# Performance work log

Measured on AMD Instinct MI355X. Metric: run time of the kernel, lower is better.

The kernel has to match this reference:

```python
import jax, jax.numpy as jnp
import numpy as np

NUM_COMPONENTS = 4
HEADS = 16


def setup_inputs() -> dict:
    key = jax.random.key(0)
    ks = jax.random.split(key, 7)
    BC, S, D = 8, 4096, 1024      # batch_times_comp = batch(2) * num_components(4)
    Se, De = 256, 2048            # encoder seq len, encoder hidden dim
    sc = 0.02                     # keep linear outputs in a sane range
    return {
        "hidden_states": jax.random.normal(ks[0], (BC, S, D), jnp.float32),
        "encoder_hidden_states": jax.random.normal(ks[1], (BC, Se, De), jnp.float32),
        "Wq": jax.random.normal(ks[2], (D, D), jnp.float32) * sc,
        "Wk": jax.random.normal(ks[3], (De, D), jnp.float32) * sc,
        "Wv": jax.random.normal(ks[4], (De, D), jnp.float32) * sc,
        "Wo": jax.random.normal(ks[5], (D, D), jnp.float32) * sc,
        "bo": jnp.zeros((D,), jnp.float32),
    }


def reference(hidden_states, encoder_hidden_states, Wq, Wk, Wv, Wo, bo):
    C, H = NUM_COMPONENTS, HEADS
    BC, S, D = hidden_states.shape
    Se = encoder_hidden_states.shape[1]
    B = BC // C
    dh = D // H
    scale = dh ** -0.5  # attn.scale (learn_temperature=False)

    # projections -> [BC, H, S(e), dh]
    q = (hidden_states @ Wq).reshape(BC, S, H, dh).transpose(0, 2, 1, 3)
    k = (encoder_hidden_states @ Wk).reshape(BC, Se, H, dh).transpose(0, 2, 1, 3)
    v = (encoder_hidden_states @ Wv).reshape(BC, Se, H, dh).transpose(0, 2, 1, 3)

    # dense scores [BC, H, S, Se]
    scores = jnp.einsum("bhsd,bhtd->bhst", q, k) * scale
    # softmax over the COMPONENT axis (dim 0 after the 5D view)
    scores5 = scores.reshape(C, B, H, S, Se)
    w = jax.nn.softmax(scores5, axis=0)  # [C, B, H, S, Se]

    # compositional (negative) entropy, summed over components -> [B, H, S, Se]
    compositional_entropy = (w * jnp.log(w)).sum(axis=0)

    # rescale and attend
    w = (w * (C / Se)).reshape(BC, H, S, Se)
    out = jnp.einsum("bhst,bhtd->bhsd", w, v)
    out = out.transpose(0, 2, 1, 3).reshape(BC, S, D)

    # to_out[0] linear (+bias), to_out[1] dropout = identity at eval,
    # residual connection, rescale_output_factor = 1
    out = out @ Wo + bo + hidden_states
    return out, compositional_entropy
```

## Files before the change

### kernel.cpp

```cpp
#include <hip/hip_runtime.h>

typedef unsigned short u16;
typedef __bf16 bf16x4 __attribute__((ext_vector_type(4)));
typedef __bf16 bf16x8 __attribute__((ext_vector_type(8)));
typedef float f32x4 __attribute__((ext_vector_type(4)));
typedef u16 u16x4 __attribute__((ext_vector_type(4)));
typedef u16 u16x8 __attribute__((ext_vector_type(8)));

#define AS1P(p) ((__attribute__((address_space(1))) void*)(unsigned long long)(p))
#define AS3P(p) ((__attribute__((address_space(3))) void*)(unsigned long long)(p))
#define MFMA16(a, b, c) __builtin_amdgcn_mfma_f32_16x16x32_bf16((a), (b), (c), 0, 0, 0)

__device__ __forceinline__ u16 f2b(float x) { return __builtin_bit_cast(u16, (__bf16)x); }
__device__ __forceinline__ float b2f(u16 u) {
  return __builtin_bit_cast(float, (unsigned)u << 16);
}

__global__ __launch_bounds__(256) void cvt_f32_bf16(const float* __restrict__ in,
                                                    u16* __restrict__ out, int n4) {
  int stride = gridDim.x * blockDim.x;
  for (int i = blockIdx.x * blockDim.x + threadIdx.x; i < n4; i += stride) {
    f32x4 v = *(const f32x4*)(in + (long)i * 4);
    u16x4 o;
    o[0] = f2b(v[0]); o[1] = f2b(v[1]); o[2] = f2b(v[2]); o[3] = f2b(v[3]);
    *(u16x4*)(out + (long)i * 4) = o;
  }
}

__global__ __launch_bounds__(256) void wtrans(const float* __restrict__ W,
                                              u16* __restrict__ Wt, int K, int N) {
  __shared__ float tile[32][33];
  int nbk = K >> 5;
  int bk = blockIdx.x % nbk;
  int bn = blockIdx.x / nbk;
  int tx = threadIdx.x & 31, ty = threadIdx.x >> 5;
#pragma unroll
  for (int i = 0; i < 32; i += 8)
    tile[ty + i][tx] = W[(long)(bk * 32 + ty + i) * N + bn * 32 + tx];
  __syncthreads();
#pragma unroll
  for (int i = 0; i < 32; i += 8)
    Wt[(long)(bn * 32 + ty + i) * K + bk * 32 + tx] = f2b(tile[tx][ty + i]);
}

__global__ __launch_bounds__(256) void vtrans(const u16* __restrict__ kvb,
                                              u16* __restrict__ vt) {
  __shared__ u16 tile[32][33];
  int bt = blockIdx.x & 7;
  int bd = (blockIdx.x >> 3) & 31;
  int bc = blockIdx.x >> 8;
  int tx = threadIdx.x & 31, ty = threadIdx.x >> 5;
  const long ob = (long)bc * 1024 * 256;
  const float RS = 1.0f / 64.0f;
#pragma unroll
  for (int i = 0; i < 32; i += 8)
    tile[ty + i][tx] =
        kvb[((long)bc * 256 + bt * 32 + ty + i) * 2048 + 1024 + bd * 32 + tx];
  __syncthreads();
#pragma unroll
  for (int i = 0; i < 32; i += 8)
    vt[ob + (long)(bd * 32 + ty + i) * 256 + bt * 32 + tx] =
        f2b(b2f(tile[tx][ty + i]) * RS);
}

__global__ __launch_bounds__(256) void kfrag_build(const u16* __restrict__ kvb,
                                                   u16* __restrict__ kfrag) {
  int wv = ((int)blockIdx.x << 2) + (threadIdx.x >> 6);
  int lane = threadIdx.x & 63, lr = lane & 15, lg = lane >> 4;
  int ks = wv & 1, tsl = (wv >> 1) & 1, c = (wv >> 2) & 3;
  int ch = (wv >> 4) & 7, h = (wv >> 7) & 15, b = (wv >> 11) & 1;
  const u16* src = kvb + ((long)(c * 2 + b) * 256 + ch * 32 + tsl * 16 + lr) * 2048 +
                   h * 64 + ks * 32 + lg * 8;
  *(bf16x8*)(kfrag + (long)wv * 512 + lane * 8) = *(const bf16x8*)src;
}

__global__ __launch_bounds__(256) void vfrag_build(const u16* __restrict__ vtb,
                                                   u16* __restrict__ vfrag) {
  int wv = ((int)blockIdx.x << 2) + (threadIdx.x >> 6);
  int lane = threadIdx.x & 63, lr = lane & 15, lg = lane >> 4;
  int dsu = wv & 3, c = (wv >> 2) & 3;
  int ch = (wv >> 4) & 7, h = (wv >> 7) & 15, b = (wv >> 11) & 1;
  const u16* src = vtb + ((long)(c * 2 + b) * 1024 + h * 64 + dsu * 16 + lr) * 256 +
                   ch * 32 + lg * 8;
  *(bf16x8*)(vfrag + (long)wv * 512 + lane * 8) = *(const bf16x8*)src;
}

__global__ __launch_bounds__(256) void gemm_bt(
    const u16* __restrict__ A, const u16* __restrict__ Bt,
    u16* __restrict__ outb, int M, int N, int K, float ascale) {
  __shared__ u16 lA[128 * 64];
  __shared__ u16 lB[128 * 64];
  const int tid = threadIdx.x;
  const int lane = tid & 63;
  const int wid = tid >> 6;
  const int wm = wid >> 1, wn = wid & 1;
  const int lr = lane & 15, lg = lane >> 4;

  int bid = (int)blockIdx.x;
  int nwg = (int)gridDim.x;
  if ((nwg & 7) == 0) bid = (bid & 7) * (nwg >> 3) + (bid >> 3);

  const int nbn = N >> 7;
  const int bm = bid / nbn;
  const int bn = bid % nbn;
  const long arow0 = (long)bm * 128;
  const long brow0 = (long)bn * 128;

  f32x4 acc[4][4] = {};

  const int srow = tid >> 3;
  const int scol = tid & 7;

  for (int k0 = 0; k0 < K; k0 += 64) {
#pragma unroll
    for (int i = 0; i < 4; ++i) {
      int row = i * 32 + srow;
      int kc = scol ^ (row & 7);
      __builtin_amdgcn_global_load_lds(AS1P(A + (arow0 + row) * K + k0 + kc * 8),
                                       AS3P(lA + i * 2048 + (tid & ~63) * 8), 16, 0, 0);
    }
#pragma unroll
    for (int i = 0; i < 4; ++i) {
      int row = i * 32 + srow;
      int kc = scol ^ (row & 7);
      __builtin_amdgcn_global_load_lds(AS1P(Bt + (brow0 + row) * K + k0 + kc * 8),
                                       AS3P(lB + i * 2048 + (tid & ~63) * 8), 16, 0, 0);
    }
    asm volatile("s_waitcnt vmcnt(0)" ::: "memory");
    __syncthreads();

#pragma unroll
    for (int ks = 0; ks < 2; ++ks) {
      bf16x8 af[4], bfr[4];
#pragma unroll
      for (int m = 0; m < 4; ++m) {
        int row = wm * 64 + m * 16 + lr;
        int off = row * 128 + ks * 64 + lg * 16;
        off ^= (row & 7) << 4;
        af[m] = *(const bf16x8*)((const char*)lA + off);
      }
#pragma unroll
      for (int n = 0; n < 4; ++n) {
        int row = wn * 64 + n * 16 + lr;
        int off = row * 128 + ks * 64 + lg * 16;
        off ^= (row & 7) << 4;
        bfr[n] = *(const bf16x8*)((const char*)lB + off);
      }
#pragma unroll
      for (int m = 0; m < 4; ++m)
#pragma unroll
        for (int n = 0; n < 4; ++n)
          acc[m][n] = MFMA16(af[m], bfr[n], acc[m][n]);
    }
    __syncthreads();
  }

#pragma unroll
  for (int m = 0; m < 4; ++m)
#pragma unroll
    for (int n = 0; n < 4; ++n) {
      long col = brow0 + wn * 64 + n * 16 + lr;
#pragma unroll
      for (int r = 0; r < 4; ++r) {
        long row = arow0 + wm * 64 + m * 16 + lg * 4 + r;
        outb[row * N + col] = f2b(acc[m][n][r] * ascale);
      }
    }
}

template <int MODE>
__global__ __launch_bounds__(512, 2) void gemm256(
    const u16* __restrict__ A, const u16* __restrict__ Bt,
    u16* __restrict__ outb, float* __restrict__ outf,
    const float* __restrict__ bias, const float* __restrict__ resid,
    int M, int N, int K, float ascale) {
  __shared__ u16 lds[2][2][256 * 64];
  const int tid = threadIdx.x;
  const int lane = tid & 63;
  const int wid = tid >> 6;
  const int wm = wid >> 2;
  const int wn = wid & 3;
  const int lr = lane & 15, lg = lane >> 4;

  int bid = (int)blockIdx.x;
  int nwg = (int)gridDim.x;
  bid = (bid & 7) * (nwg >> 3) + (bid >> 3);

  const int nbn = N >> 8;
  const int bm = bid / nbn;
  const int bn = bid % nbn;
  const long arow0 = (long)bm * 256;
  const long brow0 = (long)bn * 256;

  f32x4 acc[8][4] = {};

  const int srow = tid >> 3;
  const int scol = tid & 7;
  const int nt = K >> 6;

#define STAGE256(bf, t)                                                                \
  do {                                                                                 \
    int k0_ = (t) << 6;                                                                \
    _Pragma("unroll") for (int i = 0; i < 4; ++i) {                                    \
      int row = i * 64 + srow;                                                         \
      int kc = scol ^ (row & 7);                                                       \
      __builtin_amdgcn_global_load_lds(AS1P(A + (arow0 + row) * K + k0_ + kc * 8),     \
                                       AS3P(&lds[bf][0][0] + i * 4096 + (tid & ~63) * 8), \
                                       16, 0, 0);                                      \
    }                                                                                  \
    _Pragma("unroll") for (int i = 0; i < 4; ++i) {                                    \
      int row = i * 64 + srow;                                                         \
      int kc = scol ^ (row & 7);                                                       \
      __builtin_amdgcn_global_load_lds(AS1P(Bt + (brow0 + row) * K + k0_ + kc * 8),    \
                                       AS3P(&lds[bf][1][0] + i * 4096 + (tid & ~63) * 8), \
                                       16, 0, 0);                                      \
    }                                                                                  \
  } while (0)

#define COMPUTE256(bf)                                                                 \
  do {                                                                                 \
    _Pragma("unroll") for (int ks = 0; ks < 2; ++ks) {                                 \
      bf16x8 af[8], bfr[4];                                                            \
      _Pragma("unroll") for (int m = 0; m < 8; ++m) {                                  \
        int row = wm * 128 + m * 16 + lr;                                              \
        int off = row * 128 + ks * 64 + lg * 16;                                       \
        off ^= (row & 7) << 4;                                                         \
        af[m] = *(const bf16x8*)((const char*)&lds[bf][0][0] + off);                   \
      }                                                                                \
      _Pragma("unroll") for (int n = 0; n < 4; ++n) {                                  \
        int row = wn * 64 + n * 16 + lr;                                               \
        int off = row * 128 + ks * 64 + lg * 16;                                       \
        off ^= (row & 7) << 4;                                                         \
        bfr[n] = *(const bf16x8*)((const char*)&lds[bf][1][0] + off);                  \
      }                                                                                \
      _Pragma("unroll") for (int m = 0; m < 8; ++m)                                    \
          _Pragma("unroll") for (int n = 0; n < 4; ++n)                                \
              acc[m][n] = MFMA16(af[m], bfr[n], acc[m][n]);                            \
    }                                                                                  \
  } while (0)

  STAGE256(0, 0);
  asm volatile("s_waitcnt vmcnt(0)" ::: "memory");
  __syncthreads();
  int cur = 0;
  for (int t = 0; t < nt - 1; ++t) {
    STAGE256(cur ^ 1, t + 1);
    COMPUTE256(cur);
    asm volatile("s_waitcnt vmcnt(0)" ::: "memory");
    __syncthreads();
    cur ^= 1;
  }
  COMPUTE256(cur);

#pragma unroll
  for (int m = 0; m < 8; ++m)
#pragma unroll
    for (int n = 0; n < 4; ++n) {
      long col = brow0 + wn * 64 + n * 16 + lr;
#pragma unroll
      for (int r = 0; r < 4; ++r) {
        long row = arow0 + wm * 128 + m * 16 + lg * 4 + r;
        float v = acc[m][n][r];
        if (MODE == 1) {
          long idx = row * N + col;
          outf[idx] = v + bias[col] + resid[idx];
        } else {
          outb[row * N + col] = f2b(v * ascale);
        }
      }
    }
#undef STAGE256
#undef COMPUTE256
}

__global__ __launch_bounds__(256, 1) void attn_fused(
    const u16* __restrict__ q,
    const u16* __restrict__ kfrag,
    const u16* __restrict__ vfrag,
    u16* __restrict__ attn,
    float* __restrict__ ent) {
  const int B = 2, H = 16, S = 4096, Se = 256, D = 1024;
  __shared__ u16 ldsP[4 * 2304];
  const int tid = threadIdx.x;
  const int lane = tid & 63, wid = tid >> 6;
  const int lr = lane & 15, lg = lane >> 4;
  int bid = (int)blockIdx.x;
  bid = (bid & 7) * 256 + (bid >> 3);
  const int sblk = bid & 63;
  const int h = (bid >> 6) & 15;
  const int b = bid >> 10;
  const int s0 = sblk * 64 + wid * 16;

  u16* Pw = ldsP + wid * 2304;

  bf16x8 qf[4][2];
#pragma unroll
  for (int c = 0; c < 4; ++c)
#pragma unroll
    for (int ks = 0; ks < 2; ++ks)
      qf[c][ks] = *(const bf16x8*)(q + ((c * B + b) * (long)S + s0 + lr) * D +
                                   h * 64 + ks * 32 + lg * 8);

  const u16* kbh = kfrag + (long)(b * 16 + h) * 65536 + lane * 8;
  const u16* vbh = vfrag + (long)(b * 16 + h) * 65536 + lane * 8;
  float* entp = ent + ((long)(b * H + h) * S + s0 + lg * 4) * Se + lr;

  const float LN2 = 0.69314718056f;

  f32x4 oacc[4][4] = {};

  bf16x8 kf[16];
#pragma unroll
  for (int i = 0; i < 16; ++i) kf[i] = *(const bf16x8*)(kbh + (i << 9));

#pragma unroll
  for (int ch = 0; ch < 8; ++ch) {
    const u16* vc = vbh + ch * 8192;
    bf16x8 vf[16];
#pragma unroll
    for (int i = 0; i < 16; ++i) vf[i] = *(const bf16x8*)(vc + (i << 9));
    bf16x8 kfn[16];
    if (ch < 7) {
      const u16* kn = kbh + (ch + 1) * 8192;
#pragma unroll
      for (int i = 0; i < 16; ++i) kfn[i] = *(const bf16x8*)(kn + (i << 9));
    }
    __builtin_amdgcn_sched_barrier(0);

    f32x4 sacc[4][2] = {};
#pragma unroll
    for (int c = 0; c < 4; ++c)
#pragma unroll
      for (int tsl = 0; tsl < 2; ++tsl)
#pragma unroll
        for (int ks = 0; ks < 2; ++ks)
          sacc[c][tsl] = MFMA16(qf[c][ks], kf[c * 4 + tsl * 2 + ks], sacc[c][tsl]);

#pragma unroll
    for (int tsl = 0; tsl < 2; ++tsl) {
#pragma unroll
      for (int r = 0; r < 4; ++r) {
        float t0 = sacc[0][tsl][r];
        float t1 = sacc[1][tsl][r];
        float t2 = sacc[2][tsl][r];
        float t3 = sacc[3][tsl][r];
        float e0 = __builtin_amdgcn_exp2f(t0);
        float e1 = __builtin_amdgcn_exp2f(t1);
        float e2 = __builtin_amdgcn_exp2f(t2);
        float e3 = __builtin_amdgcn_exp2f(t3);
        float sum = (e0 + e1) + (e2 + e3);
        float inv = __builtin_amdgcn_rcpf(sum);
        float l2s = __builtin_amdgcn_logf(sum);
        float w0 = e0 * inv, w1 = e1 * inv, w2 = e2 * inv, w3 = e3 * inv;
        float entv = (w0 * t0 + w1 * t1 + w2 * t2 + w3 * t3 - l2s) * LN2;
        __builtin_nontemporal_store(entv, entp + r * Se + ch * 32 + tsl * 16);
        int pof = (lg * 4 + r) * 36 + tsl * 16 + lr;
        Pw[0 * 576 + pof] = f2b(w0);
        Pw[1 * 576 + pof] = f2b(w1);
        Pw[2 * 576 + pof] = f2b(w2);
        Pw[3 * 576 + pof] = f2b(w3);
      }
    }

#pragma unroll
    for (int c = 0; c < 4; ++c) {
      union { bf16x4 hh[2]; bf16x8 v; } pu;
      pu.hh[0] = *(const bf16x4*)(Pw + c * 576 + lr * 36 + lg * 8);
      pu.hh[1] = *(const bf16x4*)(Pw + c * 576 + lr * 36 + lg * 8 + 4);
      bf16x8 pf = pu.v;
#pragma unroll
      for (int dsu = 0; dsu < 4; ++dsu)
        oacc[c][dsu] = MFMA16(pf, vf[c * 4 + dsu], oacc[c][dsu]);
    }

    if (ch < 7) {
#pragma unroll
      for (int i = 0; i < 16; ++i) kf[i] = kfn[i];
    }
  }

#pragma unroll
  for (int c = 0; c < 4; ++c)
#pragma unroll
    for (int dsu = 0; dsu < 4; ++dsu)
#pragma unroll
      for (int r = 0; r < 4; ++r) {
        int s = s0 + lg * 4 + r;
        attn[((c * B + b) * (long)S + s) * D + h * 64 + dsu * 16 + lr] =
            f2b(oacc[c][dsu][r]);
      }
}

extern "C" void kernel_launch(void* const* d_in, const int* in_sizes, int n_in,
                              void* d_out, int out_size, void* d_ws, size_t ws_size,
                              hipStream_t stream) {
  const float* hs  = (const float*)d_in[0];
  const float* ehs = (const float*)d_in[1];
  const float* Wq  = (const float*)d_in[2];
  const float* Wk  = (const float*)d_in[3];
  const float* Wv  = (const float*)d_in[4];
  const float* Wo  = (const float*)d_in[5];
  const float* bo  = (const float*)d_in[6];
  float* out = (float*)d_out;
  float* ent = out + (size_t)8 * 4096 * 1024;

  char* ws = (char*)d_ws;
  u16* hsb   = (u16*)(ws);
  u16* ehsb  = (u16*)(ws + 67108864);
  u16* kfrag = (u16*)(ws + 67108864);
  u16* vfrag = (u16*)(ws + 71303168);
  u16* wqT   = (u16*)(ws + 75497472);
  u16* wkT   = (u16*)(ws + 77594624);
  u16* wvT   = (u16*)(ws + 81788928);
  u16* woT   = (u16*)(ws + 85983232);
  u16* qb    = (u16*)(ws + 88080384);
  u16* kvb   = (u16*)(ws + 155189248);
  u16* vtb   = (u16*)(ws + 163577856);

  const float QSCALE = 0.125f * 1.44269504f;

  cvt_f32_bf16<<<2048, 256, 0, stream>>>(hs, hsb, (8 * 4096 * 1024) / 4);
  cvt_f32_bf16<<<512, 256, 0, stream>>>(ehs, ehsb, (8 * 256 * 2048) / 4);
  wtrans<<<1024, 256, 0, stream>>>(Wq, wqT, 1024, 1024);
  wtrans<<<2048, 256, 0, stream>>>(Wk, wkT, 2048, 1024);
  wtrans<<<2048, 256, 0, stream>>>(Wv, wvT, 2048, 1024);
  wtrans<<<1024, 256, 0, stream>>>(Wo, woT, 1024, 1024);
  gemm256<0><<<(32768 / 256) * (1024 / 256), 512, 0, stream>>>(
      hsb, wqT, qb, nullptr, nullptr, nullptr, 32768, 1024, 1024, QSCALE);
  gemm_bt<<<(2048 / 128) * (2048 / 128), 256, 0, stream>>>(
      ehsb, wkT, kvb, 2048, 2048, 2048, 1.0f);
  vtrans<<<2048, 256, 0, stream>>>(kvb, vtb);
  kfrag_build<<<1024, 256, 0, stream>>>(kvb, kfrag);
  vfrag_build<<<1024, 256, 0, stream>>>(vtb, vfrag);
  attn_fused<<<2048, 256, 0, stream>>>(qb, kfrag, vfrag, hsb, ent);
  gemm256<1><<<(32768 / 256) * (1024 / 256), 512, 0, stream>>>(
      hsb, woT, nullptr, out, bo, hs, 32768, 1024, 1024, 1.0f);
}
```

Baseline: 412.8 us.

## Split gemm256 K-tiles into half-stages with finer-grained LDS pipelining

Restructures the 256x256 GEMM main loop so each 64-wide K tile is staged as two 32-wide halves in separate LDS slots. Fragments for one half are read while the next half is prefetched, and partial vmcnt waits with raw s_barrier replace the full drain and __syncthreads. MFMA bursts are also wrapped in s_setprio to favour matrix issue. The aim is to hide global-to-LDS latency inside the loop, at the cost of more barriers per tile and fragile wait-count accounting.

```diff
diff --git a/kernel.cpp b/kernel.cpp
--- a/kernel.cpp
+++ b/kernel.cpp
@@ -174,7 +174,7 @@
     u16* __restrict__ outb, float* __restrict__ outf,
     const float* __restrict__ bias, const float* __restrict__ resid,
     int M, int N, int K, float ascale) {
-  __shared__ u16 lds[2][2][256 * 64];
+  __shared__ u16 lds[2][2][2][8192];
   const int tid = threadIdx.x;
   const int lane = tid & 63;
   const int wid = tid >> 6;
@@ -193,64 +193,103 @@
   const long brow0 = (long)bn * 256;
 
   f32x4 acc[8][4] = {};
-
-  const int srow = tid >> 3;
-  const int scol = tid & 7;
   const int nt = K >> 6;
 
-#define STAGE256(bf, t)                                                                \
+  const int strow = tid >> 2;
+  const int sslot0 = tid & 3;
+
+#define STAGEH(buf, ks, t)                                                             \
   do {                                                                                 \
-    int k0_ = (t) << 6;                                                                \
-    _Pragma("unroll") for (int i = 0; i < 4; ++i) {                                    \
-      int row = i * 64 + srow;                                                         \
-      int kc = scol ^ (row & 7);                                                       \
-      __builtin_amdgcn_global_load_lds(AS1P(A + (arow0 + row) * K + k0_ + kc * 8),     \
-                                       AS3P(&lds[bf][0][0] + i * 4096 + (tid & ~63) * 8), \
-                                       16, 0, 0);                                      \
-    }                                                                                  \
-    _Pragma("unroll") for (int i = 0; i < 4; ++i) {                                    \
-      int row = i * 64 + srow;                                                         \
-      int kc = scol ^ (row & 7);                                                       \
-      __builtin_amdgcn_global_load_lds(AS1P(Bt + (brow0 + row) * K + k0_ + kc * 8),    \
-                                       AS3P(&lds[bf][1][0] + i * 4096 + (tid & ~63) * 8), \
-                                       16, 0, 0);                                      \
+    const int k0_ = ((t) << 6) + ((ks) << 5);                                          \
+    _Pragma("unroll") for (int i = 0; i < 2; ++i) {                                    \
+      int row = i * 128 + strow;                                                       \
+      int ss = sslot0 ^ (row & 3);                     \
+      __builtin_amdgcn_global_load_lds(                                                \
+          AS1P(A + (arow0 + row) * K + k0_ + ss * 8),                                  \
+          AS3P(&lds[buf][ks][0][0] + i * 4096 + (tid & ~63) * 8), 16, 0, 0);           \
+      __builtin_amdgcn_global_load_lds(                                                \
+          AS1P(Bt + (brow0 + row) * K + k0_ + ss * 8),                                 \
+          AS3P(&lds[buf][ks][1][0] + i * 4096 + (tid & ~63) * 8), 16, 0, 0);           \
     }                                                                                  \
   } while (0)
 
-#define COMPUTE256(bf)                                                                 \
+#define LOADFRAGS(buf, ks)                                                             \
   do {                                                                                 \
-    _Pragma("unroll") for (int ks = 0; ks < 2; ++ks) {                                 \
-      bf16x8 af[8], bfr[4];                                                            \
-      _Pragma("unroll") for (int m = 0; m < 8; ++m) {                                  \
-        int row = wm * 128 + m * 16 + lr;                                              \
-        int off = row * 128 + ks * 64 + lg * 16;                                       \
-        off ^= (row & 7) << 4;                                                         \
-        af[m] = *(const bf16x8*)((const char*)&lds[bf][0][0] + off);                   \
-      }                                                                                \
-      _Pragma("unroll") for (int n = 0; n < 4; ++n) {                                  \
-        int row = wn * 64 + n * 16 + lr;                                               \
-        int off = row * 128 + ks * 64 + lg * 16;                                       \
-        off ^= (row & 7) << 4;                                                         \
-        bfr[n] = *(const bf16x8*)((const char*)&lds[bf][1][0] + off);                  \
-      }                                                                                \
-      _Pragma("unroll") for (int m = 0; m < 8; ++m)                                    \
-          _Pragma("unroll") for (int n = 0; n < 4; ++n)                                \
-              acc[m][n] = MFMA16(af[m], bfr[n], acc[m][n]);                            \
+    const u16* bA = &lds[buf][ks][0][0];                                               \
+    const u16* bB = &lds[buf][ks][1][0];                                               \
+    _Pragma("unroll") for (int m = 0; m < 8; ++m) {                                    \
+      int row = wm * 128 + m * 16 + lr;                                                \
+      af[m] = *(const bf16x8*)(bA + row * 32 + (lg ^ (row & 3)) * 8);                  \
+    }                                                                                  \
+    _Pragma("unroll") for (int n = 0; n < 4; ++n) {                                    \
+      int row = wn * 64 + n * 16 + lr;                                                 \
+      bfr[n] = *(const bf16x8*)(bB + row * 32 + (lg ^ (row & 3)) * 8);                 \
     }                                                                                  \
   } while (0)
 
-  STAGE256(0, 0);
-  asm volatile("s_waitcnt vmcnt(0)" ::: "memory");
-  __syncthreads();
-  int cur = 0;
+#define DOMFMA()                                                                       \
+  do {                                                                                 \
+    __builtin_amdgcn_s_setprio(1);                                                     \
+    _Pragma("unroll") for (int m = 0; m < 8; ++m)                                      \
+        _Pragma("unroll") for (int n = 0; n < 4; ++n)                                  \
+            acc[m][n] = MFMA16(af[m], bfr[n], acc[m][n]);                              \
+    __builtin_amdgcn_s_setprio(0);                                                     \
+  } while (0)
+
+  STAGEH(0, 0, 0);
+  STAGEH(0, 1, 0);
+  STAGEH(1, 0, 1);
+  asm volatile("s_waitcnt vmcnt(8)" ::: "memory");
+  __builtin_amdgcn_s_barrier();
+  __builtin_amdgcn_sched_barrier(0);
+
   for (int t = 0; t < nt - 1; ++t) {
-    STAGE256(cur ^ 1, t + 1);
-    COMPUTE256(cur);
-    asm volatile("s_waitcnt vmcnt(0)" ::: "memory");
-    __syncthreads();
-    cur ^= 1;
+    const int cb = t & 1, nb = cb ^ 1;
+    {
+      bf16x8 af[8], bfr[4];
+      LOADFRAGS(cb, 0);
+      STAGEH(nb, 1, t + 1);
+      asm volatile("s_waitcnt vmcnt(8)" ::: "memory");
+      __builtin_amdgcn_s_barrier();
+      __builtin_amdgcn_sched_barrier(0);
+      DOMFMA();
+      __builtin_amdgcn_s_barrier();
+      __builtin_amdgcn_sched_barrier(0);
+    }
+    {
+      bf16x8 af[8], bfr[4];
+      LOADFRAGS(cb, 1);
+      if (t + 2 < nt) {
+        STAGEH(cb, 0, t + 2);
+        asm volatile("s_waitcnt vmcnt(8)" ::: "memory");
+      } else {
+        asm volatile("s_waitcnt vmcnt(4)" ::: "memory");
+      }
+      __builtin_amdgcn_s_barrier();
+      __builtin_amdgcn_sched_barrier(0);
+      DOMFMA();
+      __builtin_amdgcn_s_barrier();
+      __builtin_amdgcn_sched_barrier(0);
+    }
   }
-  COMPUTE256(cur);
+  {
+    const int cb = (nt - 1) & 1;
+    {
+      bf16x8 af[8], bfr[4];
+      LOADFRAGS(cb, 0);
+      asm volatile("s_waitcnt vmcnt(0)" ::: "memory");
+      __builtin_amdgcn_s_barrier();
+      __builtin_amdgcn_sched_barrier(0);
+      DOMFMA();
+      __builtin_amdgcn_s_barrier();
+      __builtin_amdgcn_sched_barrier(0);
+    }
+    {
+      bf16x8 af[8], bfr[4];
+      LOADFRAGS(cb, 1);
+      DOMFMA();
+    }
+  }
 
 #pragma unroll
   for (int m = 0; m < 8; ++m)
@@ -269,8 +308,9 @@
         }
       }
     }
-#undef STAGE256
-#undef COMPUTE256
+#undef STAGEH
+#undef LOADFRAGS
+#undef DOMFMA
 }
 
 __global__ __launch_bounds__(256, 1) void attn_fused(
```

Measured after the change: 420.1 us. No clear change (+1.8%).

## Double-buffer K/V fragments in attention and read residual from bf16 copy

Applied to the files above, without the earlier changes.

The attention kernel now prefetches both the K and V fragments of the next chunk into ping-pong register buffers, through a fully unrolled macro, instead of loading V for the current chunk just before use. The goal is to hide V load latency behind the score and softmax work. The output projection now reads the residual from the bf16 copy of hidden_states instead of the fp32 input, which halves that read traffic, and it stores the fp32 output with nontemporal stores. Attention output is written in place over the q buffer. The trade-offs are much higher register pressure in the attention kernel and lower precision in the residual add.

```diff
diff --git a/kernel.cpp b/kernel.cpp
--- a/kernel.cpp
+++ b/kernel.cpp
@@ -172,7 +172,7 @@
 __global__ __launch_bounds__(512, 2) void gemm256(
     const u16* __restrict__ A, const u16* __restrict__ Bt,
     u16* __restrict__ outb, float* __restrict__ outf,
-    const float* __restrict__ bias, const float* __restrict__ resid,
+    const float* __restrict__ bias, const u16* __restrict__ residb,
     int M, int N, int K, float ascale) {
   __shared__ u16 lds[2][2][256 * 64];
   const int tid = threadIdx.x;
@@ -263,7 +263,7 @@
         float v = acc[m][n][r];
         if (MODE == 1) {
           long idx = row * N + col;
-          outf[idx] = v + bias[col] + resid[idx];
+          __builtin_nontemporal_store(v + bias[col] + b2f(residb[idx]), outf + idx);
         } else {
           outb[row * N + col] = f2b(v * ascale);
         }
@@ -274,10 +274,10 @@
 }
 
 __global__ __launch_bounds__(256, 1) void attn_fused(
-    const u16* __restrict__ q,
+    const u16* q,
     const u16* __restrict__ kfrag,
     const u16* __restrict__ vfrag,
-    u16* __restrict__ attn,
+    u16* attnout,
     float* __restrict__ ent) {
   const int B = 2, H = 16, S = 4096, Se = 256, D = 1024;
   __shared__ u16 ldsP[4 * 2304];
@@ -309,75 +309,71 @@
 
   f32x4 oacc[4][4] = {};
 
-  bf16x8 kf[16];
-#pragma unroll
-  for (int i = 0; i < 16; ++i) kf[i] = *(const bf16x8*)(kbh + (i << 9));
-
-#pragma unroll
-  for (int ch = 0; ch < 8; ++ch) {
-    const u16* vc = vbh + ch * 8192;
-    bf16x8 vf[16];
-#pragma unroll
-    for (int i = 0; i < 16; ++i) vf[i] = *(const bf16x8*)(vc + (i << 9));
-    bf16x8 kfn[16];
-    if (ch < 7) {
-      const u16* kn = kbh + (ch + 1) * 8192;
-#pragma unroll
-      for (int i = 0; i < 16; ++i) kfn[i] = *(const bf16x8*)(kn + (i << 9));
-    }
-    __builtin_amdgcn_sched_barrier(0);
-
-    f32x4 sacc[4][2] = {};
-#pragma unroll
-    for (int c = 0; c < 4; ++c)
-#pragma unroll
-      for (int tsl = 0; tsl < 2; ++tsl)
-#pragma unroll
-        for (int ks = 0; ks < 2; ++ks)
-          sacc[c][tsl] = MFMA16(qf[c][ks], kf[c * 4 + tsl * 2 + ks], sacc[c][tsl]);
-
-#pragma unroll
-    for (int tsl = 0; tsl < 2; ++tsl) {
-#pragma unroll
-      for (int r = 0; r < 4; ++r) {
-        float t0 = sacc[0][tsl][r];
-        float t1 = sacc[1][tsl][r];
-        float t2 = sacc[2][tsl][r];
-        float t3 = sacc[3][tsl][r];
-        float e0 = __builtin_amdgcn_exp2f(t0);
-        float e1 = __builtin_amdgcn_exp2f(t1);
-        float e2 = __builtin_amdgcn_exp2f(t2);
-        float e3 = __builtin_amdgcn_exp2f(t3);
-        float sum = (e0 + e1) + (e2 + e3);
-        float inv = __builtin_amdgcn_rcpf(sum);
-        float l2s = __builtin_amdgcn_logf(sum);
-        float w0 = e0 * inv, w1 = e1 * inv, w2 = e2 * inv, w3 = e3 * inv;
-        float entv = (w0 * t0 + w1 * t1 + w2 * t2 + w3 * t3 - l2s) * LN2;
-        __builtin_nontemporal_store(entv, entp + r * Se + ch * 32 + tsl * 16);
-        int pof = (lg * 4 + r) * 36 + tsl * 16 + lr;
-        Pw[0 * 576 + pof] = f2b(w0);
-        Pw[1 * 576 + pof] = f2b(w1);
-        Pw[2 * 576 + pof] = f2b(w2);
-        Pw[3 * 576 + pof] = f2b(w3);
-      }
-    }
-
-#pragma unroll
-    for (int c = 0; c < 4; ++c) {
-      union { bf16x4 hh[2]; bf16x8 v; } pu;
-      pu.hh[0] = *(const bf16x4*)(Pw + c * 576 + lr * 36 + lg * 8);
-      pu.hh[1] = *(const bf16x4*)(Pw + c * 576 + lr * 36 + lg * 8 + 4);
-      bf16x8 pf = pu.v;
-#pragma unroll
-      for (int dsu = 0; dsu < 4; ++dsu)
-        oacc[c][dsu] = MFMA16(pf, vf[c * 4 + dsu], oacc[c][dsu]);
-    }
-
-    if (ch < 7) {
-#pragma unroll
-      for (int i = 0; i < 16; ++i) kf[i] = kfn[i];
-    }
+  bf16x8 kf0[16], kf1[16], vf0[16], vf1[16];
+#pragma unroll
+  for (int i = 0; i < 16; ++i) kf0[i] = *(const bf16x8*)(kbh + (i << 9));
+#pragma unroll
+  for (int i = 0; i < 16; ++i) vf0[i] = *(const bf16x8*)(vbh + (i << 9));
+
+#define ATTN_CHUNK(CH, KFC, VFC, KFN, VFN, LAST)                                       \
+  {                                                                                    \
+    if (!(LAST)) {                                                                     \
+      const u16* kn = kbh + ((CH) + 1) * 8192;                                         \
+      _Pragma("unroll") for (int i = 0; i < 16; ++i)                                   \
+          KFN[i] = *(const bf16x8*)(kn + (i << 9));                                    \
+      const u16* vn = vbh + ((CH) + 1) * 8192;                                         \
+      _Pragma("unroll") for (int i = 0; i < 16; ++i)                                   \
+          VFN[i] = *(const bf16x8*)(vn + (i << 9));                                    \
+    }                                                                                  \
+    __builtin_amdgcn_sched_barrier(0);                                                 \
+    f32x4 sacc[4][2] = {};                                                             \
+    _Pragma("unroll") for (int c = 0; c < 4; ++c)                                      \
+        _Pragma("unroll") for (int tsl = 0; tsl < 2; ++tsl)                            \
+            _Pragma("unroll") for (int ks = 0; ks < 2; ++ks)                           \
+                sacc[c][tsl] =                                                         \
+                    MFMA16(qf[c][ks], KFC[c * 4 + tsl * 2 + ks], sacc[c][tsl]);        \
+    _Pragma("unroll") for (int tsl = 0; tsl < 2; ++tsl) {                              \
+      _Pragma("unroll") for (int r = 0; r < 4; ++r) {                                  \
+        float t0 = sacc[0][tsl][r];                                                    \
+        float t1 = sacc[1][tsl][r];                                                    \
+        float t2 = sacc[2][tsl][r];                                                    \
+        float t3 = sacc[3][tsl][r];                                                    \
+        float e0 = __builtin_amdgcn_exp2f(t0);                                         \
+        float e1 = __builtin_amdgcn_exp2f(t1);                                         \
+        float e2 = __builtin_amdgcn_exp2f(t2);                                         \
+        float e3 = __builtin_amdgcn_exp2f(t3);                                         \
+        float sum = (e0 + e1) + (e2 + e3);                                             \
+        float inv = __builtin_amdgcn_rcpf(sum);                                        \
+        float l2s = __builtin_amdgcn_logf(sum);                                        \
+        float w0 = e0 * inv, w1 = e1 * inv, w2 = e2 * inv, w3 = e3 * inv;              \
+        float entv = (w0 * t0 + w1 * t1 + w2 * t2 + w3 * t3 - l2s) * LN2;              \
+        __builtin_nontemporal_store(entv, entp + r * Se + (CH) * 32 + tsl * 16);       \
+        int pof = (lg * 4 + r) * 36 + tsl * 16 + lr;                                   \
+        Pw[0 * 576 + pof] = f2b(w0);                                                   \
+        Pw[1 * 576 + pof] = f2b(w1);                                                   \
+        Pw[2 * 576 + pof] = f2b(w2);                                                   \
+        Pw[3 * 576 + pof] = f2b(w3);                                                   \
+      }                                                                                \
+    }                                                                                  \
+    _Pragma("unroll") for (int c = 0; c < 4; ++c) {                                    \
+      union { bf16x4 hh[2]; bf16x8 v; } pu;                                            \
+      pu.hh[0] = *(const bf16x4*)(Pw + c * 576 + lr * 36 + lg * 8);                    \
+      pu.hh[1] = *(const bf16x4*)(Pw + c * 576 + lr * 36 + lg * 8 + 4);                \
+      bf16x8 pf = pu.v;                                                                \
+      _Pragma("unroll") for (int dsu = 0; dsu < 4; ++dsu)                              \
+          oacc[c][dsu] = MFMA16(pf, VFC[c * 4 + dsu], oacc[c][dsu]);                   \
+    }                                                                                  \
   }
+
+  ATTN_CHUNK(0, kf0, vf0, kf1, vf1, false)
+  ATTN_CHUNK(1, kf1, vf1, kf0, vf0, false)
+  ATTN_CHUNK(2, kf0, vf0, kf1, vf1, false)
+  ATTN_CHUNK(3, kf1, vf1, kf0, vf0, false)
+  ATTN_CHUNK(4, kf0, vf0, kf1, vf1, false)
+  ATTN_CHUNK(5, kf1, vf1, kf0, vf0, false)
+  ATTN_CHUNK(6, kf0, vf0, kf1, vf1, false)
+  ATTN_CHUNK(7, kf1, vf1, kf0, vf0, true)
+#undef ATTN_CHUNK
 
 #pragma unroll
   for (int c = 0; c < 4; ++c)
@@ -386,7 +382,7 @@
 #pragma unroll
       for (int r = 0; r < 4; ++r) {
         int s = s0 + lg * 4 + r;
-        attn[((c * B + b) * (long)S + s) * D + h * 64 + dsu * 16 + lr] =
+        attnout[((c * B + b) * (long)S + s) * D + h * 64 + dsu * 16 + lr] =
             f2b(oacc[c][dsu][r]);
       }
 }
@@ -432,7 +428,7 @@
   vtrans<<<2048, 256, 0, stream>>>(kvb, vtb);
   kfrag_build<<<1024, 256, 0, stream>>>(kvb, kfrag);
   vfrag_build<<<1024, 256, 0, stream>>>(vtb, vfrag);
-  attn_fused<<<2048, 256, 0, stream>>>(qb, kfrag, vfrag, hsb, ent);
+  attn_fused<<<2048, 256, 0, stream>>>(qb, kfrag, vfrag, qb, ent);
   gemm256<1><<<(32768 / 256) * (1024 / 256), 512, 0, stream>>>(
-      hsb, woT, nullptr, out, bo, hs, 32768, 1024, 1024, 1.0f);
-}
+      qb, woT, nullptr, out, bo, hsb, 32768, 1024, 1024, 1.0f);
+}
```

New measurement: 463.3 us. 1.12x slower.
